# Kernel tuning notes

Measured on AMD Instinct MI355X. Metric: run time of the kernel, lower is better.

## Reference

```python
import jax, jax.numpy as jnp
import numpy as np
from jax import lax

CHUNK = 64
KEY_DIM = 128
SCALE = KEY_DIM ** -0.5  # query scaling
EPS = 1e-06


def setup_inputs() -> dict:
    key = jax.random.key(0)
    ks = jax.random.split(key, 5)
    B, H, S, Dk, Dv = 2, 16, 4096, 128, 256
    q = jax.random.normal(ks[0], (B, H, S, Dk), jnp.float32)
    k = jax.random.normal(ks[1], (B, H, S, Dk), jnp.float32)
    v = jax.random.normal(ks[2], (B, H, S, Dv), jnp.float32)
    # decay log-gate: small negative values
    g = -0.1 * jax.random.uniform(ks[3], (B, H, S), jnp.float32)
    # delta-rule learning rate in (0, 1)
    beta = 0.05 + 0.9 * jax.random.uniform(ks[4], (B, H, S), jnp.float32)
    return {"q": q, "k": k, "v": v, "g": g, "beta": beta}


def _chunkwise(q, k, v, g, beta):
    B, H, S, Dk = q.shape
    Dv = v.shape[-1]
    L = CHUNK
    N = S // L  # S chosen as multiple of CHUNK (pad branch is a no-op)
    # L2-normalize q, k
    q = q / (jnp.linalg.norm(q, axis=-1, keepdims=True) + EPS)
    k = k / (jnp.linalg.norm(k, axis=-1, keepdims=True) + EPS)
    # chunk and move chunk axis to front for scan: [N, B, H, L, D]
    qc = jnp.transpose(q.reshape(B, H, N, L, Dk), (2, 0, 1, 3, 4))
    kc = jnp.transpose(k.reshape(B, H, N, L, Dk), (2, 0, 1, 3, 4))
    vc = jnp.transpose(v.reshape(B, H, N, L, Dv), (2, 0, 1, 3, 4))
    gc = jnp.transpose(g.reshape(B, H, N, L), (2, 0, 1, 3))
    bc = jnp.transpose(beta.reshape(B, H, N, L), (2, 0, 1, 3))

    eye = jnp.eye(L, dtype=jnp.float32)
    mask_lower = jnp.tril(jnp.ones((L, L), jnp.float32), k=-1)
    causal_mask = jnp.tril(jnp.ones((L, L), jnp.float32))

    def process_chunk(S_state, chunk_inputs):
        q_c, k_c, v_c, g_c, beta_c = chunk_inputs
        g_cum = jnp.cumsum(g_c, axis=-1)                     # [B,H,L]
        g_total = g_cum[..., -1]                             # [B,H]
        relative_gate = jnp.exp(g_cum[..., None, :] - g_cum[..., :, None])  # [B,H,L,L]
        kk = jnp.einsum('bhik,bhjk->bhij', k_c, k_c)
        M = kk * relative_gate * mask_lower
        A = eye + beta_c[..., None] * M
        diag_beta = eye * beta_c[..., None]
        T = lax.linalg.triangular_solve(A, diag_beta, left_side=True, lower=True)
        g_cum_exp = jnp.exp(g_cum)[..., None]                # [B,H,L,1]
        k_gated = k_c * g_cum_exp
        v_gated = v_c * g_cum_exp
        W = jnp.einsum('bhij,bhjk->bhik', T, k_gated)
        U = jnp.einsum('bhij,bhjv->bhiv', T, v_gated)
        O_inter = jnp.einsum('bhik,bhkv->bhiv', q_c, S_state) * g_cum_exp
        WS = jnp.einsum('bhik,bhkv->bhiv', W, S_state)
        correction = U - WS
        qk = jnp.einsum('bhik,bhjk->bhij', q_c, k_c)
        qk_gated = qk * causal_mask * relative_gate
        O_intra = jnp.einsum('bhij,bhjv->bhiv', qk_gated * SCALE, correction)
        O_chunk = O_inter * SCALE + O_intra
        S_new = S_state * jnp.exp(g_total)[..., None, None] + \
            jnp.einsum('bhik,bhiv->bhkv', k_gated, correction)
        return S_new, O_chunk

    S0 = jnp.zeros((B, H, Dk, Dv), dtype=jnp.float32)
    final_state, outputs = lax.scan(process_chunk, S0, (qc, kc, vc, gc, bc))
    output = jnp.transpose(outputs, (1, 2, 0, 3, 4)).reshape(B, H, S, Dv)
    return output.astype(q.dtype), final_state


def reference(q, k, v, g, beta):
    return _chunkwise(q, k, v, g, beta)
```

## Files before the change

### kernel.cpp

```cpp
#include <hip/hip_runtime.h>
#include <math.h>


namespace {

constexpr int kBH = 32;
constexpr int kS = 4096;
constexpr int kDk = 128;
constexpr int kDv = 256;
constexpr int kL = 64;
constexpr int kNC = kS / kL;
constexpr int kThreads = 512;
constexpr float kScale = 0.08838834764831845f;
constexpr float kEps = 1e-6f;

constexpr int KST = 136;
constexpr int TST = 72;
constexpr int SBT = 136;
constexpr int AS  = 68;

typedef __attribute__((ext_vector_type(8))) short short8;
typedef __attribute__((ext_vector_type(4))) short short4v;
typedef __attribute__((ext_vector_type(4))) float f32x4;

__device__ __forceinline__ short f2bf(float f) {
  union { float f; unsigned u; } x;
  x.f = f;
  unsigned r = x.u + 0x7fffu + ((x.u >> 16) & 1u);
  return (short)(r >> 16);
}

#define MFMA16(a, b, c) __builtin_amdgcn_mfma_f32_16x16x32_bf16((a), (b), (c), 0, 0, 0)

__global__ __launch_bounds__(kThreads, 2)
void gdn_mfma_kernel(const float* __restrict__ q, const float* __restrict__ k,
                     const float* __restrict__ v, const float* __restrict__ g,
                     const float* __restrict__ beta, float* __restrict__ out) {
  __shared__ short sKp[kL][KST];
  __shared__ short sKm[kL][KST];
  __shared__ short sQp[kL][KST];
  __shared__ short sQm[kL][KST];
  __shared__ short sTb[kL][TST];
  __shared__ short sAqk[kL][TST];
  __shared__ short sSb[32][SBT];
  __shared__ short sYT[32][TST];
  __shared__ short sCT[32][TST];
  __shared__ float sA[kL][AS];
  __shared__ float sVinv[4][16][17];
  __shared__ float sTmp[32][33];
  __shared__ float sGexp[kL], sGinv[kL], sBeta[kL];

  const int t = threadIdx.x;
  const int wave = t >> 6;
  const int lane = t & 63;
  const int n16 = lane & 15;
  const int quad = lane >> 4;
  const int r2 = t >> 3;
  const int c8 = t & 7;

  const int bh = blockIdx.x & 31;
  const int vb = blockIdx.x >> 5;

  const float* qp_g = q + (size_t)bh * kS * kDk;
  const float* kp_g = k + (size_t)bh * kS * kDk;
  const float* vp_g = v + (size_t)bh * kS * kDv + vb * 32;
  const float* gp_g = g + (size_t)bh * kS;
  const float* bp_g = beta + (size_t)bh * kS;
  float* op_g = out + (size_t)bh * kS * kDv + vb * 32;
  float* sp_g = out + (size_t)kBH * kS * kDv + (size_t)bh * kDk * kDv + vb * 32;

  for (int i = t; i < kL * TST; i += kThreads) { (&sTb[0][0])[i] = 0; (&sAqk[0][0])[i] = 0; }
  for (int i = t; i < 32 * SBT; i += kThreads) (&sSb[0][0])[i] = 0;

  f32x4 Sacc[4];
  Sacc[0] = 0; Sacc[1] = 0; Sacc[2] = 0; Sacc[3] = 0;

  for (int n = 0; n < kNC; ++n) {
    __syncthreads();

    float kv[16], qv[16], rk, rq;
    {
      const float* krow = kp_g + (size_t)(n * kL + r2) * kDk + c8 * 16;
      const float* qrow = qp_g + (size_t)(n * kL + r2) * kDk + c8 * 16;
      float ssk = 0.f, ssq = 0.f;
      #pragma unroll
      for (int m = 0; m < 4; ++m) {
        const float4 a = reinterpret_cast<const float4*>(krow)[m];
        const float4 b = reinterpret_cast<const float4*>(qrow)[m];
        kv[4*m+0]=a.x; kv[4*m+1]=a.y; kv[4*m+2]=a.z; kv[4*m+3]=a.w;
        qv[4*m+0]=b.x; qv[4*m+1]=b.y; qv[4*m+2]=b.z; qv[4*m+3]=b.w;
        ssk += a.x*a.x + a.y*a.y + a.z*a.z + a.w*a.w;
        ssq += b.x*b.x + b.y*b.y + b.z*b.z + b.w*b.w;
      }
      #pragma unroll
      for (int off = 4; off >= 1; off >>= 1) {
        ssk += __shfl_xor(ssk, off, 8);
        ssq += __shfl_xor(ssq, off, 8);
      }
      rk = 1.f / (sqrtf(ssk) + kEps);
      rq = 1.f / (sqrtf(ssq) + kEps);
    }
    if (t < kL) {
      float gv = gp_g[n * kL + t];
      float bt = bp_g[n * kL + t];
      #pragma unroll
      for (int off = 1; off < 64; off <<= 1) {
        float up = __shfl_up(gv, off, 64);
        if (lane >= off) gv += up;
      }
      sGexp[t] = __expf(gv);
      sGinv[t] = __expf(-gv);
      sBeta[t] = bt;
    }
    __syncthreads();

    {
      const float ge = sGexp[r2], gi = sGinv[r2];
      const float m_kp = rk * ge, m_km = rk * gi;
      const float m_qp = rq * ge * kScale, m_qm = rq * gi * kScale;
      short8 w0, w1;
      #pragma unroll
      for (int m = 0; m < 8; ++m) { w0[m] = f2bf(kv[m] * m_kp); w1[m] = f2bf(kv[8+m] * m_kp); }
      *(short8*)&sKp[r2][c8*16] = w0; *(short8*)&sKp[r2][c8*16+8] = w1;
      #pragma unroll
      for (int m = 0; m < 8; ++m) { w0[m] = f2bf(kv[m] * m_km); w1[m] = f2bf(kv[8+m] * m_km); }
      *(short8*)&sKm[r2][c8*16] = w0; *(short8*)&sKm[r2][c8*16+8] = w1;
      #pragma unroll
      for (int m = 0; m < 8; ++m) { w0[m] = f2bf(qv[m] * m_qp); w1[m] = f2bf(qv[8+m] * m_qp); }
      *(short8*)&sQp[r2][c8*16] = w0; *(short8*)&sQp[r2][c8*16+8] = w1;
      #pragma unroll
      for (int m = 0; m < 8; ++m) { w0[m] = f2bf(qv[m] * m_qm); w1[m] = f2bf(qv[8+m] * m_qm); }
      *(short8*)&sQm[r2][c8*16] = w0; *(short8*)&sQm[r2][c8*16+8] = w1;
    }
    __syncthreads();

    {
      const int jmax = wave & 3;
      const int i0 = (wave & 3) * 16;
      const short (*Asrc)[KST] = (wave < 4) ? sKm : sQm;
      f32x4 acc[4];
      acc[0] = 0; acc[1] = 0; acc[2] = 0; acc[3] = 0;
      #pragma unroll
      for (int ks = 0; ks < 4; ++ks) {
        short8 af = *(const short8*)&Asrc[i0 + n16][ks*32 + quad*8];
        for (int jt = 0; jt <= jmax; ++jt) {
          short8 bf = *(const short8*)&sKp[jt*16 + n16][ks*32 + quad*8];
          acc[jt] = MFMA16(af, bf, acc[jt]);
        }
      }
      if (wave < 4) {
        #pragma unroll
        for (int reg = 0; reg < 4; ++reg) {
          const int i = i0 + quad*4 + reg;
          const float bi = sBeta[i];
          for (int jt = 0; jt <= jmax; ++jt) {
            const int j = jt*16 + n16;
            if (j < i) sA[i][j] = bi * acc[jt][reg];
          }
        }
      } else {
        for (int jt = 0; jt <= jmax; ++jt) {
          #pragma unroll
          for (int reg = 0; reg < 4; ++reg) {
            const int i = i0 + quad*4 + reg, j = jt*16 + n16;
            sAqk[i][j] = (j <= i) ? f2bf(acc[jt][reg]) : (short)0;
          }
        }
      }
    }
    __syncthreads();

    f32x4 yacc[2], oacc[2];
    float vv[2][4];
    const int iy0 = (wave & 3) * 16;
    auto py_step = [&](int ks) {
      short8 ak = *(const short8*)&sKp[iy0 + n16][ks*32 + quad*8];
      short8 aq = *(const short8*)&sQp[iy0 + n16][ks*32 + quad*8];
      #pragma unroll
      for (int vt = 0; vt < 2; ++vt) {
        short8 bs = *(const short8*)&sSb[vt*16 + n16][ks*32 + quad*8];
        yacc[vt] = MFMA16(ak, bs, yacc[vt]);
        oacc[vt] = MFMA16(aq, bs, oacc[vt]);
      }
    };

    if (wave >= 4) {
      yacc[0] = 0; yacc[1] = 0; oacc[0] = 0; oacc[1] = 0;
      #pragma unroll
      for (int vt = 0; vt < 2; ++vt)
        #pragma unroll
        for (int reg = 0; reg < 4; ++reg)
          vv[vt][reg] = vp_g[(size_t)(n*kL + iy0 + quad*4 + reg) * kDv + vt*16 + n16];
      py_step(0);
    } else if (t < 64) {
      const int I = t >> 4, c = t & 15;
      float x[16];
      #pragma unroll
      for (int i = 0; i < 16; ++i) {
        float xi = (i == c) ? 1.f : 0.f;
        for (int j = 0; j < i; ++j) xi -= sA[I*16 + i][I*16 + j] * x[j];
        x[i] = xi;
      }
      const float bc = sBeta[I*16 + c];
      #pragma unroll
      for (int i = 0; i < 16; ++i) {
        sVinv[I][i][c] = x[i];
        sTb[I*16 + i][I*16 + c] = f2bf(x[i] * bc);
      }
    }
    __syncthreads();

    if (wave >= 4) {
      py_step(1);
    } else {
      const int r = t >> 4, c = t & 15;
      float m1 = 0.f, m3 = 0.f;
      #pragma unroll
      for (int kk = 0; kk < 16; ++kk) {
        m1 += sVinv[1][r][kk] * sA[16 + kk][c];
        m3 += sVinv[3][r][kk] * sA[48 + kk][32 + c];
      }
      sTmp[r][c] = m1;
      sTmp[16 + r][c] = m3;
    }
    __syncthreads();

    if (wave >= 4) {
      py_step(2);
    } else {
      const int r = t >> 4, c = t & 15;
      float x1 = 0.f, x3 = 0.f;
      #pragma unroll
      for (int kk = 0; kk < 16; ++kk) {
        x1 += sTmp[r][kk] * sVinv[0][kk][c];
        x3 += sTmp[16 + r][kk] * sVinv[2][kk][c];
      }
      x1 = -x1; x3 = -x3;
      sA[16 + r][c] = x1;
      sTb[16 + r][c] = f2bf(x1 * sBeta[c]);
      sA[48 + r][32 + c] = x3;
      sTb[48 + r][32 + c] = f2bf(x3 * sBeta[32 + c]);
    }
    __syncthreads();

    if (wave >= 4) {
      py_step(3);
    } else {
      #pragma unroll
      for (int p = 0; p < 4; ++p) {
        const int idx = t + 256*p;
        const int r = idx >> 5, c = idx & 31;
        float m = 0.f;
        if (c < 16) {
          #pragma unroll
          for (int kk = 0; kk < 16; ++kk) m += sA[32 + r][kk] * sVinv[0][kk][c];
          #pragma unroll
          for (int kk = 16; kk < 32; ++kk) m += sA[32 + r][kk] * sA[kk][c];
        } else {
          #pragma unroll
          for (int kk = 16; kk < 32; ++kk) m += sA[32 + r][kk] * sVinv[1][kk - 16][c - 16];
        }
        sTmp[r][c] = m;
      }
    }
    __syncthreads();

    if (wave >= 4) {
      #pragma unroll
      for (int vt = 0; vt < 2; ++vt) {
        short4v yw;
        #pragma unroll
        for (int reg = 0; reg < 4; ++reg) {
          const float gei = sGexp[iy0 + quad*4 + reg];
          yw[reg] = f2bf(gei * vv[vt][reg] - yacc[vt][reg]);
        }
        *(short4v*)&sYT[vt*16 + n16][iy0 + quad*4] = yw;
      }
    } else {
      #pragma unroll
      for (int p = 0; p < 4; ++p) {
        const int idx = t + 256*p;
        const int r = idx >> 5, c = idx & 31;
        float xv = 0.f;
        if (r < 16) {
          #pragma unroll
          for (int kk = 0; kk < 16; ++kk) xv += sVinv[2][r][kk] * sTmp[kk][c];
        } else {
          #pragma unroll
          for (int kk = 0; kk < 16; ++kk) xv += sA[32 + r][32 + kk] * sTmp[kk][c];
          #pragma unroll
          for (int kk = 16; kk < 32; ++kk) xv += sVinv[3][r - 16][kk - 16] * sTmp[kk][c];
        }
        sTb[32 + r][c] = f2bf(-xv * sBeta[c]);
      }
    }
    __syncthreads();

    {
      const int ic0 = (wave >> 1) * 16, vc0 = (wave & 1) * 16;
      f32x4 cacc; cacc = 0;
      #pragma unroll
      for (int ks = 0; ks < 2; ++ks) {
        short8 af = *(const short8*)&sTb[ic0 + n16][ks*32 + quad*8];
        short8 bf = *(const short8*)&sYT[vc0 + n16][ks*32 + quad*8];
        cacc = MFMA16(af, bf, cacc);
      }
      short4v cw;
      #pragma unroll
      for (int reg = 0; reg < 4; ++reg) cw[reg] = f2bf(cacc[reg]);
      *(short4v*)&sCT[vc0 + n16][ic0 + quad*4] = cw;
    }
    __syncthreads();

    if (wave >= 4) {
      const int io = (wave & 3) * 16;
      #pragma unroll
      for (int ks = 0; ks < 2; ++ks) {
        short8 af = *(const short8*)&sAqk[io + n16][ks*32 + quad*8];
        #pragma unroll
        for (int vt = 0; vt < 2; ++vt) {
          short8 bf = *(const short8*)&sCT[vt*16 + n16][ks*32 + quad*8];
          oacc[vt] = MFMA16(af, bf, oacc[vt]);
        }
      }
      #pragma unroll
      for (int vt = 0; vt < 2; ++vt)
        #pragma unroll
        for (int reg = 0; reg < 4; ++reg)
          op_g[(size_t)(n*kL + io + quad*4 + reg) * kDv + vt*16 + n16] = oacc[vt][reg];
    } else {
      const float decay = sGexp[kL - 1];
      Sacc[0] *= decay; Sacc[1] *= decay; Sacc[2] *= decay; Sacc[3] *= decay;
      #pragma unroll
      for (int a = 0; a < 2; ++a) {
        const int d0 = (wave & 3) * 32 + a * 16;
        #pragma unroll
        for (int ks = 0; ks < 2; ++ks) {
          short8 af;
          #pragma unroll
          for (int j = 0; j < 8; ++j) af[j] = sKp[ks*32 + quad*8 + j][d0 + n16];
          #pragma unroll
          for (int b = 0; b < 2; ++b) {
            short8 bf = *(const short8*)&sCT[b*16 + n16][ks*32 + quad*8];
            Sacc[a*2 + b] = MFMA16(af, bf, Sacc[a*2 + b]);
          }
        }
        #pragma unroll
        for (int b = 0; b < 2; ++b) {
          short4v sw;
          #pragma unroll
          for (int reg = 0; reg < 4; ++reg) sw[reg] = f2bf(Sacc[a*2 + b][reg]);
          *(short4v*)&sSb[b*16 + n16][d0 + quad*4] = sw;
        }
      }
    }
  }

  if (wave < 4) {
    #pragma unroll
    for (int a = 0; a < 2; ++a)
      #pragma unroll
      for (int b = 0; b < 2; ++b)
        #pragma unroll
        for (int reg = 0; reg < 4; ++reg) {
          const int d = (wave & 3) * 32 + a * 16 + quad * 4 + reg;
          sp_g[(size_t)d * kDv + b * 16 + n16] = Sacc[a*2 + b][reg];
        }
  }
}

}

extern "C" void kernel_launch(void* const* d_in, const int* in_sizes, int n_in,
                              void* d_out, int out_size, void* d_ws, size_t ws_size,
                              hipStream_t stream) {
  (void)in_sizes; (void)n_in; (void)d_ws; (void)ws_size; (void)out_size;
  const float* q    = (const float*)d_in[0];
  const float* k    = (const float*)d_in[1];
  const float* v    = (const float*)d_in[2];
  const float* g    = (const float*)d_in[3];
  const float* beta = (const float*)d_in[4];
  float* out = (float*)d_out;
  gdn_mfma_kernel<<<dim3(kBH * (kDv / 32)), dim3(kThreads), 0, stream>>>(
      q, k, v, g, beta, out);
}
```

Baseline: 957.0 us.

## Prefetch next chunk's q/k/g/beta and fold gating into products

Loads the next chunk's q, k, g and beta into registers during the current chunk and computes its norms and gate cumsum early, using double-buffered gate/beta arrays in shared memory. The four gated bf16 copies of q and k collapse to two plain normalized copies, with the exp(±g) gating applied to the MFMA results (A, Aqk, Y, C, output) instead. The v load also moves earlier. Together these hide global-load latency, drop two shared stores per chunk and free shared memory, at the cost of more registers and different bf16 rounding points.

```diff
diff --git a/kernel.cpp b/kernel.cpp
--- a/kernel.cpp
+++ b/kernel.cpp
@@ -36,19 +36,19 @@
 void gdn_mfma_kernel(const float* __restrict__ q, const float* __restrict__ k,
                      const float* __restrict__ v, const float* __restrict__ g,
                      const float* __restrict__ beta, float* __restrict__ out) {
-  __shared__ short sKp[kL][KST];
-  __shared__ short sKm[kL][KST];
-  __shared__ short sQp[kL][KST];
-  __shared__ short sQm[kL][KST];
-  __shared__ short sTb[kL][TST];
-  __shared__ short sAqk[kL][TST];
-  __shared__ short sSb[32][SBT];
-  __shared__ short sYT[32][TST];
-  __shared__ short sCT[32][TST];
-  __shared__ float sA[kL][AS];
-  __shared__ float sVinv[4][16][17];
-  __shared__ float sTmp[32][33];
-  __shared__ float sGexp[kL], sGinv[kL], sBeta[kL];
+  __shared__ __align__(16) short sKn[kL][KST];
+  __shared__ __align__(16) short sQn[kL][KST];
+  __shared__ __align__(16) short sTb[kL][TST];
+  __shared__ __align__(16) short sAqk[kL][TST];
+  __shared__ __align__(16) short sSb[32][SBT];
+  __shared__ __align__(16) float sA[kL][AS];
+  __shared__ __align__(16) float sVinv[4][16][17];
+  __shared__ __align__(16) float sTmp[32][33];
+  __shared__ __align__(16) short sYT[32][TST];
+  __shared__ __align__(16) short sCT[32][TST];
+  __shared__ __align__(16) float sGe[2][kL];
+  __shared__ __align__(16) float sGi[2][kL];
+  __shared__ __align__(16) float sBeta[2][kL];
 
   const int t = threadIdx.x;
   const int wave = t >> 6;
@@ -57,6 +57,7 @@
   const int quad = lane >> 4;
   const int r2 = t >> 3;
   const int c8 = t & 7;
+  const int iy0 = (wave & 3) * 16;
 
   const int bh = blockIdx.x & 31;
   const int vb = blockIdx.x >> 5;
@@ -75,95 +76,136 @@
   f32x4 Sacc[4];
   Sacc[0] = 0; Sacc[1] = 0; Sacc[2] = 0; Sacc[3] = 0;
 
-  for (int n = 0; n < kNC; ++n) {
-    __syncthreads();
-
-    float kv[16], qv[16], rk, rq;
-    {
-      const float* krow = kp_g + (size_t)(n * kL + r2) * kDk + c8 * 16;
-      const float* qrow = qp_g + (size_t)(n * kL + r2) * kDk + c8 * 16;
-      float ssk = 0.f, ssq = 0.f;
-      #pragma unroll
-      for (int m = 0; m < 4; ++m) {
-        const float4 a = reinterpret_cast<const float4*>(krow)[m];
-        const float4 b = reinterpret_cast<const float4*>(qrow)[m];
-        kv[4*m+0]=a.x; kv[4*m+1]=a.y; kv[4*m+2]=a.z; kv[4*m+3]=a.w;
-        qv[4*m+0]=b.x; qv[4*m+1]=b.y; qv[4*m+2]=b.z; qv[4*m+3]=b.w;
-        ssk += a.x*a.x + a.y*a.y + a.z*a.z + a.w*a.w;
-        ssq += b.x*b.x + b.y*b.y + b.z*b.z + b.w*b.w;
-      }
-      #pragma unroll
-      for (int off = 4; off >= 1; off >>= 1) {
-        ssk += __shfl_xor(ssk, off, 8);
-        ssq += __shfl_xor(ssq, off, 8);
-      }
-      rk = 1.f / (sqrtf(ssk) + kEps);
-      rq = 1.f / (sqrtf(ssq) + kEps);
-    }
+  float4 kv4[4], qv4[4];
+  float gv0 = 0.f, bt0 = 0.f;
+  float krk = 0.f, krq = 0.f;
+
+  {
+    const float* krow = kp_g + (size_t)r2 * kDk + c8 * 16;
+    const float* qrow = qp_g + (size_t)r2 * kDk + c8 * 16;
+    #pragma unroll
+    for (int m = 0; m < 4; ++m) {
+      kv4[m] = reinterpret_cast<const float4*>(krow)[m];
+      qv4[m] = reinterpret_cast<const float4*>(qrow)[m];
+    }
+    if (t < kL) { gv0 = gp_g[t]; bt0 = bp_g[t]; }
+    float ssk = 0.f, ssq = 0.f;
+    #pragma unroll
+    for (int m = 0; m < 4; ++m) {
+      ssk += kv4[m].x * kv4[m].x + kv4[m].y * kv4[m].y +
+             kv4[m].z * kv4[m].z + kv4[m].w * kv4[m].w;
+      ssq += qv4[m].x * qv4[m].x + qv4[m].y * qv4[m].y +
+             qv4[m].z * qv4[m].z + qv4[m].w * qv4[m].w;
+    }
+    #pragma unroll
+    for (int off = 4; off >= 1; off >>= 1) {
+      ssk += __shfl_xor(ssk, off, 8);
+      ssq += __shfl_xor(ssq, off, 8);
+    }
+    krk = 1.f / (sqrtf(ssk) + kEps);
+    krq = kScale / (sqrtf(ssq) + kEps);
     if (t < kL) {
-      float gv = gp_g[n * kL + t];
-      float bt = bp_g[n * kL + t];
+      float gv = gv0;
       #pragma unroll
       for (int off = 1; off < 64; off <<= 1) {
         float up = __shfl_up(gv, off, 64);
         if (lane >= off) gv += up;
       }
-      sGexp[t] = __expf(gv);
-      sGinv[t] = __expf(-gv);
-      sBeta[t] = bt;
-    }
+      sGe[0][t] = __expf(gv);
+      sGi[0][t] = __expf(-gv);
+      sBeta[0][t] = bt0;
+    }
+  }
+
+  for (int n = 0; n < kNC; ++n) {
+    const int cb = n & 1;
     __syncthreads();
 
     {
-      const float ge = sGexp[r2], gi = sGinv[r2];
-      const float m_kp = rk * ge, m_km = rk * gi;
-      const float m_qp = rq * ge * kScale, m_qm = rq * gi * kScale;
-      short8 w0, w1;
-      #pragma unroll
-      for (int m = 0; m < 8; ++m) { w0[m] = f2bf(kv[m] * m_kp); w1[m] = f2bf(kv[8+m] * m_kp); }
-      *(short8*)&sKp[r2][c8*16] = w0; *(short8*)&sKp[r2][c8*16+8] = w1;
-      #pragma unroll
-      for (int m = 0; m < 8; ++m) { w0[m] = f2bf(kv[m] * m_km); w1[m] = f2bf(kv[8+m] * m_km); }
-      *(short8*)&sKm[r2][c8*16] = w0; *(short8*)&sKm[r2][c8*16+8] = w1;
-      #pragma unroll
-      for (int m = 0; m < 8; ++m) { w0[m] = f2bf(qv[m] * m_qp); w1[m] = f2bf(qv[8+m] * m_qp); }
-      *(short8*)&sQp[r2][c8*16] = w0; *(short8*)&sQp[r2][c8*16+8] = w1;
-      #pragma unroll
-      for (int m = 0; m < 8; ++m) { w0[m] = f2bf(qv[m] * m_qm); w1[m] = f2bf(qv[8+m] * m_qm); }
-      *(short8*)&sQm[r2][c8*16] = w0; *(short8*)&sQm[r2][c8*16+8] = w1;
-    }
-    __syncthreads();
-
+      const float mk = krk, mq = krq;
+      #pragma unroll
+      for (int m = 0; m < 2; ++m) {
+        const float4 a = kv4[2 * m], b2 = kv4[2 * m + 1];
+        short8 w;
+        w[0] = f2bf(a.x * mk);  w[1] = f2bf(a.y * mk);
+        w[2] = f2bf(a.z * mk);  w[3] = f2bf(a.w * mk);
+        w[4] = f2bf(b2.x * mk); w[5] = f2bf(b2.y * mk);
+        w[6] = f2bf(b2.z * mk); w[7] = f2bf(b2.w * mk);
+        *(short8*)&sKn[r2][c8 * 16 + m * 8] = w;
+      }
+      #pragma unroll
+      for (int m = 0; m < 2; ++m) {
+        const float4 a = qv4[2 * m], b2 = qv4[2 * m + 1];
+        short8 w;
+        w[0] = f2bf(a.x * mq);  w[1] = f2bf(a.y * mq);
+        w[2] = f2bf(a.z * mq);  w[3] = f2bf(a.w * mq);
+        w[4] = f2bf(b2.x * mq); w[5] = f2bf(b2.y * mq);
+        w[6] = f2bf(b2.z * mq); w[7] = f2bf(b2.w * mq);
+        *(short8*)&sQn[r2][c8 * 16 + m * 8] = w;
+      }
+    }
+    if (n + 1 < kNC) {
+      const float* krow = kp_g + (size_t)((n + 1) * kL + r2) * kDk + c8 * 16;
+      const float* qrow = qp_g + (size_t)((n + 1) * kL + r2) * kDk + c8 * 16;
+      #pragma unroll
+      for (int m = 0; m < 4; ++m) {
+        kv4[m] = reinterpret_cast<const float4*>(krow)[m];
+        qv4[m] = reinterpret_cast<const float4*>(qrow)[m];
+      }
+      if (t < kL) {
+        gv0 = gp_g[(n + 1) * kL + t];
+        bt0 = bp_g[(n + 1) * kL + t];
+      }
+    }
+    __syncthreads();
+
+    float vv[2][4];
     {
       const int jmax = wave & 3;
-      const int i0 = (wave & 3) * 16;
-      const short (*Asrc)[KST] = (wave < 4) ? sKm : sQm;
+      const short (*Asrc)[KST] = (wave < 4) ? sKn : sQn;
       f32x4 acc[4];
       acc[0] = 0; acc[1] = 0; acc[2] = 0; acc[3] = 0;
+      if (wave >= 4) {
+        #pragma unroll
+        for (int vt = 0; vt < 2; ++vt)
+          #pragma unroll
+          for (int reg = 0; reg < 4; ++reg)
+            vv[vt][reg] = vp_g[(size_t)(n * kL + iy0 + quad * 4 + reg) * kDv +
+                               vt * 16 + n16];
+      }
       #pragma unroll
       for (int ks = 0; ks < 4; ++ks) {
-        short8 af = *(const short8*)&Asrc[i0 + n16][ks*32 + quad*8];
+        short8 af = *(const short8*)&Asrc[iy0 + n16][ks * 32 + quad * 8];
         for (int jt = 0; jt <= jmax; ++jt) {
-          short8 bf = *(const short8*)&sKp[jt*16 + n16][ks*32 + quad*8];
+          short8 bf = *(const short8*)&sKn[jt * 16 + n16][ks * 32 + quad * 8];
           acc[jt] = MFMA16(af, bf, acc[jt]);
         }
       }
       if (wave < 4) {
+        float sc[4];
         #pragma unroll
         for (int reg = 0; reg < 4; ++reg) {
-          const int i = i0 + quad*4 + reg;
-          const float bi = sBeta[i];
-          for (int jt = 0; jt <= jmax; ++jt) {
-            const int j = jt*16 + n16;
-            if (j < i) sA[i][j] = bi * acc[jt][reg];
+          const int i = iy0 + quad * 4 + reg;
+          sc[reg] = sBeta[cb][i] * sGi[cb][i];
+        }
+        for (int jt = 0; jt <= jmax; ++jt) {
+          const int j = jt * 16 + n16;
+          const float gej = sGe[cb][j];
+          #pragma unroll
+          for (int reg = 0; reg < 4; ++reg) {
+            const int i = iy0 + quad * 4 + reg;
+            if (j < i) sA[i][j] = sc[reg] * gej * acc[jt][reg];
           }
         }
       } else {
+        float gi4[4];
+        #pragma unroll
+        for (int reg = 0; reg < 4; ++reg) gi4[reg] = sGi[cb][iy0 + quad * 4 + reg];
         for (int jt = 0; jt <= jmax; ++jt) {
           #pragma unroll
           for (int reg = 0; reg < 4; ++reg) {
-            const int i = i0 + quad*4 + reg, j = jt*16 + n16;
-            sAqk[i][j] = (j <= i) ? f2bf(acc[jt][reg]) : (short)0;
+            const int i = iy0 + quad * 4 + reg, j = jt * 16 + n16;
+            sAqk[i][j] = (j <= i) ? f2bf(acc[jt][reg] * gi4[reg]) : (short)0;
           }
         }
       }
@@ -171,14 +213,12 @@
     __syncthreads();
 
     f32x4 yacc[2], oacc[2];
-    float vv[2][4];
-    const int iy0 = (wave & 3) * 16;
     auto py_step = [&](int ks) {
-      short8 ak = *(const short8*)&sKp[iy0 + n16][ks*32 + quad*8];
-      short8 aq = *(const short8*)&sQp[iy0 + n16][ks*32 + quad*8];
+      short8 ak = *(const short8*)&sKn[iy0 + n16][ks * 32 + quad * 8];
+      short8 aq = *(const short8*)&sQn[iy0 + n16][ks * 32 + quad * 8];
       #pragma unroll
       for (int vt = 0; vt < 2; ++vt) {
-        short8 bs = *(const short8*)&sSb[vt*16 + n16][ks*32 + quad*8];
+        short8 bs = *(const short8*)&sSb[vt * 16 + n16][ks * 32 + quad * 8];
         yacc[vt] = MFMA16(ak, bs, yacc[vt]);
         oacc[vt] = MFMA16(aq, bs, oacc[vt]);
       }
@@ -186,11 +226,6 @@
 
     if (wave >= 4) {
       yacc[0] = 0; yacc[1] = 0; oacc[0] = 0; oacc[1] = 0;
-      #pragma unroll
-      for (int vt = 0; vt < 2; ++vt)
-        #pragma unroll
-        for (int reg = 0; reg < 4; ++reg)
-          vv[vt][reg] = vp_g[(size_t)(n*kL + iy0 + quad*4 + reg) * kDv + vt*16 + n16];
       py_step(0);
     } else if (t < 64) {
       const int I = t >> 4, c = t & 15;
@@ -198,14 +233,14 @@
       #pragma unroll
       for (int i = 0; i < 16; ++i) {
         float xi = (i == c) ? 1.f : 0.f;
-        for (int j = 0; j < i; ++j) xi -= sA[I*16 + i][I*16 + j] * x[j];
+        for (int j = 0; j < i; ++j) xi -= sA[I * 16 + i][I * 16 + j] * x[j];
         x[i] = xi;
       }
-      const float bc = sBeta[I*16 + c];
+      const float bc = sBeta[cb][I * 16 + c];
       #pragma unroll
       for (int i = 0; i < 16; ++i) {
         sVinv[I][i][c] = x[i];
-        sTb[I*16 + i][I*16 + c] = f2bf(x[i] * bc);
+        sTb[I * 16 + i][I * 16 + c] = f2bf(x[i] * bc);
       }
     }
     __syncthreads();
@@ -237,9 +272,9 @@
       }
       x1 = -x1; x3 = -x3;
       sA[16 + r][c] = x1;
-      sTb[16 + r][c] = f2bf(x1 * sBeta[c]);
+      sTb[16 + r][c] = f2bf(x1 * sBeta[cb][c]);
       sA[48 + r][32 + c] = x3;
-      sTb[48 + r][32 + c] = f2bf(x3 * sBeta[32 + c]);
+      sTb[48 + r][32 + c] = f2bf(x3 * sBeta[cb][32 + c]);
     }
     __syncthreads();
 
@@ -248,7 +283,7 @@
     } else {
       #pragma unroll
       for (int p = 0; p < 4; ++p) {
-        const int idx = t + 256*p;
+        const int idx = t + 256 * p;
         const int r = idx >> 5, c = idx & 31;
         float m = 0.f;
         if (c < 16) {
@@ -258,7 +293,8 @@
           for (int kk = 16; kk < 32; ++kk) m += sA[32 + r][kk] * sA[kk][c];
         } else {
           #pragma unroll
-          for (int kk = 16; kk < 32; ++kk) m += sA[32 + r][kk] * sVinv[1][kk - 16][c - 16];
+          for (int kk = 16; kk < 32; ++kk)
+            m += sA[32 + r][kk] * sVinv[1][kk - 16][c - 16];
         }
         sTmp[r][c] = m;
       }
@@ -271,15 +307,16 @@
         short4v yw;
         #pragma unroll
         for (int reg = 0; reg < 4; ++reg) {
-          const float gei = sGexp[iy0 + quad*4 + reg];
-          yw[reg] = f2bf(gei * vv[vt][reg] - yacc[vt][reg]);
-        }
-        *(short4v*)&sYT[vt*16 + n16][iy0 + quad*4] = yw;
+          const float ge = sGe[cb][iy0 + quad * 4 + reg];
+          yw[reg] = f2bf(ge * (vv[vt][reg] - yacc[vt][reg]));
+          oacc[vt][reg] *= ge;
+        }
+        *(short4v*)&sYT[vt * 16 + n16][iy0 + quad * 4] = yw;
       }
     } else {
       #pragma unroll
       for (int p = 0; p < 4; ++p) {
-        const int idx = t + 256*p;
+        const int idx = t + 256 * p;
         const int r = idx >> 5, c = idx & 31;
         float xv = 0.f;
         if (r < 16) {
@@ -289,9 +326,10 @@
           #pragma unroll
           for (int kk = 0; kk < 16; ++kk) xv += sA[32 + r][32 + kk] * sTmp[kk][c];
           #pragma unroll
-          for (int kk = 16; kk < 32; ++kk) xv += sVinv[3][r - 16][kk - 16] * sTmp[kk][c];
-        }
-        sTb[32 + r][c] = f2bf(-xv * sBeta[c]);
+          for (int kk = 16; kk < 32; ++kk)
+            xv += sVinv[3][r - 16][kk - 16] * sTmp[kk][c];
+        }
+        sTb[32 + r][c] = f2bf(-xv * sBeta[cb][c]);
       }
     }
     __syncthreads();
@@ -301,14 +339,43 @@
       f32x4 cacc; cacc = 0;
       #pragma unroll
       for (int ks = 0; ks < 2; ++ks) {
-        short8 af = *(const short8*)&sTb[ic0 + n16][ks*32 + quad*8];
-        short8 bf = *(const short8*)&sYT[vc0 + n16][ks*32 + quad*8];
+        short8 af = *(const short8*)&sTb[ic0 + n16][ks * 32 + quad * 8];
+        short8 bf = *(const short8*)&sYT[vc0 + n16][ks * 32 + quad * 8];
         cacc = MFMA16(af, bf, cacc);
       }
       short4v cw;
       #pragma unroll
-      for (int reg = 0; reg < 4; ++reg) cw[reg] = f2bf(cacc[reg]);
-      *(short4v*)&sCT[vc0 + n16][ic0 + quad*4] = cw;
+      for (int reg = 0; reg < 4; ++reg)
+        cw[reg] = f2bf(cacc[reg] * sGe[cb][ic0 + quad * 4 + reg]);
+      *(short4v*)&sCT[vc0 + n16][ic0 + quad * 4] = cw;
+    }
+    if (n + 1 < kNC) {
+      float ssk = 0.f, ssq = 0.f;
+      #pragma unroll
+      for (int m = 0; m < 4; ++m) {
+        ssk += kv4[m].x * kv4[m].x + kv4[m].y * kv4[m].y +
+               kv4[m].z * kv4[m].z + kv4[m].w * kv4[m].w;
+        ssq += qv4[m].x * qv4[m].x + qv4[m].y * qv4[m].y +
+               qv4[m].z * qv4[m].z + qv4[m].w * qv4[m].w;
+      }
+      #pragma unroll
+      for (int off = 4; off >= 1; off >>= 1) {
+        ssk += __shfl_xor(ssk, off, 8);
+        ssq += __shfl_xor(ssq, off, 8);
+      }
+      krk = 1.f / (sqrtf(ssk) + kEps);
+      krq = kScale / (sqrtf(ssq) + kEps);
+      if (t < kL) {
+        float gv = gv0;
+        #pragma unroll
+        for (int off = 1; off < 64; off <<= 1) {
+          float up = __shfl_up(gv, off, 64);
+          if (lane >= off) gv += up;
+        }
+        sGe[cb ^ 1][t] = __expf(gv);
+        sGi[cb ^ 1][t] = __expf(-gv);
+        sBeta[cb ^ 1][t] = bt0;
+      }
     }
     __syncthreads();
 
@@ -316,10 +383,10 @@
       const int io = (wave & 3) * 16;
       #pragma unroll
       for (int ks = 0; ks < 2; ++ks) {
-        short8 af = *(const short8*)&sAqk[io + n16][ks*32 + quad*8];
+        short8 af = *(const short8*)&sAqk[io + n16][ks * 32 + quad * 8];
         #pragma unroll
         for (int vt = 0; vt < 2; ++vt) {
-          short8 bf = *(const short8*)&sCT[vt*16 + n16][ks*32 + quad*8];
+          short8 bf = *(const short8*)&sCT[vt * 16 + n16][ks * 32 + quad * 8];
           oacc[vt] = MFMA16(af, bf, oacc[vt]);
         }
       }
@@ -327,9 +394,10 @@
       for (int vt = 0; vt < 2; ++vt)
         #pragma unroll
         for (int reg = 0; reg < 4; ++reg)
-          op_g[(size_t)(n*kL + io + quad*4 + reg) * kDv + vt*16 + n16] = oacc[vt][reg];
+          op_g[(size_t)(n * kL + io + quad * 4 + reg) * kDv + vt * 16 + n16] =
+              oacc[vt][reg];
     } else {
-      const float decay = sGexp[kL - 1];
+      const float decay = sGe[cb][kL - 1];
       Sacc[0] *= decay; Sacc[1] *= decay; Sacc[2] *= decay; Sacc[3] *= decay;
       #pragma unroll
       for (int a = 0; a < 2; ++a) {
@@ -338,19 +406,19 @@
         for (int ks = 0; ks < 2; ++ks) {
           short8 af;
           #pragma unroll
-          for (int j = 0; j < 8; ++j) af[j] = sKp[ks*32 + quad*8 + j][d0 + n16];
+          for (int j = 0; j < 8; ++j) af[j] = sKn[ks * 32 + quad * 8 + j][d0 + n16];
           #pragma unroll
           for (int b = 0; b < 2; ++b) {
-            short8 bf = *(const short8*)&sCT[b*16 + n16][ks*32 + quad*8];
-            Sacc[a*2 + b] = MFMA16(af, bf, Sacc[a*2 + b]);
+            short8 bf = *(const short8*)&sCT[b * 16 + n16][ks * 32 + quad * 8];
+            Sacc[a * 2 + b] = MFMA16(af, bf, Sacc[a * 2 + b]);
           }
         }
         #pragma unroll
         for (int b = 0; b < 2; ++b) {
           short4v sw;
           #pragma unroll
-          for (int reg = 0; reg < 4; ++reg) sw[reg] = f2bf(Sacc[a*2 + b][reg]);
-          *(short4v*)&sSb[b*16 + n16][d0 + quad*4] = sw;
+          for (int reg = 0; reg < 4; ++reg) sw[reg] = f2bf(Sacc[a * 2 + b][reg]);
+          *(short4v*)&sSb[b * 16 + n16][d0 + quad * 4] = sw;
         }
       }
     }
@@ -364,7 +432,7 @@
         #pragma unroll
         for (int reg = 0; reg < 4; ++reg) {
           const int d = (wave & 3) * 32 + a * 16 + quad * 4 + reg;
-          sp_g[(size_t)d * kDv + b * 16 + n16] = Sacc[a*2 + b][reg];
+          sp_g[(size_t)d * kDv + b * 16 + n16] = Sacc[a * 2 + b][reg];
         }
   }
 }
```

Result: faster. 933.4 us (-2.5%).
